# Performance work log

Measured on AMD Instinct MI355X. Metric: run time of the kernel, lower is better.

## Reference

```python
import jax, jax.numpy as jnp
import numpy as np

N_HEADS = 16


def setup_inputs() -> dict:
    key = jax.random.key(0)
    ks = jax.random.split(key, 5)
    B, T, C = 4, 2048, 1024
    return {
        "x": jax.random.normal(ks[0], (B, T, C), dtype=jnp.float32),
        "W_qkv": jax.random.normal(ks[1], (C, 3 * C), dtype=jnp.float32) * 0.02,
        "b_qkv": jax.random.normal(ks[2], (3 * C,), dtype=jnp.float32) * 0.02,
        "W_proj": jax.random.normal(ks[3], (C, C), dtype=jnp.float32) * 0.02,
        "b_proj": jax.random.normal(ks[4], (C,), dtype=jnp.float32) * 0.02,
    }


def reference(x, W_qkv, b_qkv, W_proj, b_proj):
    B, T, C = x.shape
    H = N_HEADS
    hs = C // H
    # QKV projection. NOTE: original reshapes (B,T,3C) -> (B,T,H,3*hs) then
    # chunks last dim, so q/k/v are interleaved per-head slices of the output.
    qkv = x @ W_qkv + b_qkv                       # [B, T, 3C]
    qkv = qkv.reshape(B, T, H, 3 * hs).transpose(0, 2, 1, 3)  # [B, H, T, 3*hs]
    q, k, v = jnp.split(qkv, 3, axis=-1)          # each [B, H, T, hs]
    scale = 1.0 / (hs ** 0.5)
    scores = jnp.einsum("bhqd,bhkd->bhqk", q, k) * scale  # [B, H, T, T]
    causal = jnp.tril(jnp.ones((T, T), dtype=bool))
    scores = jnp.where(causal, scores, jnp.float32(-1e9))
    attn = jax.nn.softmax(scores, axis=-1)
    out = jnp.einsum("bhqk,bhkd->bhqd", attn, v)  # [B, H, T, hs]
    out = out.transpose(0, 2, 1, 3).reshape(B, T, C)
    return out @ W_proj + b_proj
```

## Files before the change

### kernel.cpp

```cpp
#include <hip/hip_runtime.h>

typedef unsigned short u16;
typedef unsigned int u32;
typedef __attribute__((ext_vector_type(8))) short short8;
typedef __attribute__((ext_vector_type(8))) unsigned short u16x8;
typedef __attribute__((ext_vector_type(4))) unsigned short u16x4;
typedef __attribute__((ext_vector_type(2))) unsigned int u32x2;
typedef __attribute__((ext_vector_type(4))) float f32x4;

__device__ __forceinline__ u16 f2bf(float f){
  u32 u = __builtin_bit_cast(u32, f);
  u32 r = u + 0x7FFFu + ((u >> 16) & 1u);
  return (u16)(r >> 16);
}
__device__ __forceinline__ float bf2f(u16 h){
  u32 u = ((u32)h) << 16;
  return __builtin_bit_cast(float, u);
}
__device__ __forceinline__ float f3max(float a, float b, float c){
  return fmaxf(a, fmaxf(b, c));
}
__device__ __forceinline__ u32 cvtpk(float lo, float hi){
  u32 r;
  asm("v_cvt_pk_bf16_f32 %0, %1, %2" : "=v"(r) : "v"(lo), "v"(hi));
  return r;
}

__device__ __forceinline__ void gld_lds16(const u16* g, u16* l){
  __builtin_amdgcn_global_load_lds(
      (const __attribute__((address_space(1))) u32*)g,
      (__attribute__((address_space(3))) u32*)l, 16, 0, 0);
}

#define MFMA(a,b,c) __builtin_amdgcn_mfma_f32_16x16x32_bf16((a),(b),(c),0,0,0)

__global__ void k_cast_x(const float* __restrict__ in, u16* __restrict__ out, int n8){
  int i = blockIdx.x*256 + threadIdx.x;
  if (i >= n8) return;
  const float4 a = ((const float4*)in)[2*i];
  const float4 b = ((const float4*)in)[2*i+1];
  u16x8 o;
  o[0]=f2bf(a.x); o[1]=f2bf(a.y); o[2]=f2bf(a.z); o[3]=f2bf(a.w);
  o[4]=f2bf(b.x); o[5]=f2bf(b.y); o[6]=f2bf(b.z); o[7]=f2bf(b.w);
  ((u16x8*)out)[i] = o;
}

__global__ void k_transpose_cast(const float* __restrict__ in, u16* __restrict__ out,
                                 int R, int C){
  __shared__ float tile[32][33];
  int c0 = blockIdx.x*32, r0 = blockIdx.y*32;
  int tx = threadIdx.x, ty = threadIdx.y;
  #pragma unroll
  for (int i=0;i<4;i++) tile[ty+8*i][tx] = in[(size_t)(r0+ty+8*i)*C + c0+tx];
  __syncthreads();
  #pragma unroll
  for (int i=0;i<4;i++) out[(size_t)(c0+ty+8*i)*R + r0+tx] = f2bf(tile[tx][ty+8*i]);
}

template<int OUT_BF16>
__global__ __launch_bounds__(256) void gemm_bt(const u16* __restrict__ A,
                                               const u16* __restrict__ Bt,
                                               const float* __restrict__ bias,
                                               void* __restrict__ Cp,
                                               int M, int N, int K){
  __shared__ __align__(16) u16 As[128*32];
  __shared__ __align__(16) u16 Bs[128*32];
  int tid = threadIdx.x, lane = tid&63, wv = tid>>6;
  int wr = wv>>1, wc = wv&1;
  int lr16 = lane&15, lg = lane>>4;
  int nwg = gridDim.x*gridDim.y;
  int lin = blockIdx.y*gridDim.x + blockIdx.x;
  int cpx = nwg>>3;
  int swz = (lin&7)*cpx + (lin>>3);
  int bx = swz % gridDim.x, by = swz / gridDim.x;
  size_t brow = (size_t)by*128, bcol = (size_t)bx*128;
  f32x4 acc[4][4] = {};
  int nk = K>>5;
  for (int kt=0; kt<nk; ++kt){
    int k0 = kt*32;
    #pragma unroll
    for (int c=0;c<2;c++){
      gld_lds16(A  + (brow + c*64 + (tid>>2))*K + k0 + (tid&3)*8, &As[c*2048 + tid*8]);
      gld_lds16(Bt + (bcol + c*64 + (tid>>2))*K + k0 + (tid&3)*8, &Bs[c*2048 + tid*8]);
    }
    __syncthreads();
    short8 af[4], bfr[4];
    #pragma unroll
    for (int m=0;m<4;m++) af[m]  = *(const short8*)&As[(wr*64 + m*16 + lr16)*32 + lg*8];
    #pragma unroll
    for (int n=0;n<4;n++) bfr[n] = *(const short8*)&Bs[(wc*64 + n*16 + lr16)*32 + lg*8];
    #pragma unroll
    for (int m=0;m<4;m++)
      #pragma unroll
      for (int n=0;n<4;n++) acc[m][n] = MFMA(af[m], bfr[n], acc[m][n]);
    __syncthreads();
  }
  #pragma unroll
  for (int n=0;n<4;n++){
    size_t col = bcol + wc*64 + n*16 + lr16;
    float bs = bias[col];
    #pragma unroll
    for (int m=0;m<4;m++)
      #pragma unroll
      for (int j=0;j<4;j++){
        size_t row = brow + wr*64 + m*16 + lg*4 + j;
        float v = acc[m][n][j] + bs;
        if (OUT_BF16) ((u16*)Cp)[row*(size_t)N + col] = f2bf(v);
        else          ((float*)Cp)[row*(size_t)N + col] = v;
      }
  }
}

#define G_STAGE(PTR, BROW, LDS, T_, BUF) do{                                   \
  size_t k0_ = (size_t)(T_)*64;                                                \
  _Pragma("unroll")                                                            \
  for (int l=0;l<4;l++){                                                       \
    int r_ = (l&1)*64 + (tid>>3);                                              \
    int h_ = l>>1;                                                             \
    gld_lds16(PTR + (size_t)((BROW) + h_*128 + r_)*1024 + k0_ + (((tid&7)^(r_&7))*8), \
              &LDS[(BUF)*16384 + h_*8192 + (l&1)*4096 + tid*8]);               \
  }                                                                            \
}while(0)

#define RD_A(MQ, CUR) do{                                                      \
  _Pragma("unroll")                                                            \
  for (int m=0;m<4;m++)                                                        \
    _Pragma("unroll")                                                          \
    for (int k=0;k<2;k++){                                                     \
      int hr = (MQ)*64 + m*16 + lr16;                                          \
      af[m][k] = *(const short8*)&Alds[(CUR)*16384 + wr*8192 + hr*64 + (((k*4+lg)^(hr&7))*8)]; \
    }                                                                          \
}while(0)

#define RD_B(NQ, CUR) do{                                                      \
  _Pragma("unroll")                                                            \
  for (int n=0;n<2;n++)                                                        \
    _Pragma("unroll")                                                          \
    for (int k=0;k<2;k++){                                                     \
      int hr = (wc&1)*64 + ((NQ)*2+n)*16 + lr16;                               \
      bfv[(NQ)*2+n][k] = *(const short8*)&Blds[(CUR)*16384 + (wc>>1)*8192 + hr*64 + (((k*4+lg)^(hr&7))*8)]; \
    }                                                                          \
}while(0)

#define MF16(MQ, NQ)                                                           \
  _Pragma("unroll")                                                            \
  for (int k=0;k<2;k++)                                                        \
    _Pragma("unroll")                                                          \
    for (int m=0;m<4;m++)                                                      \
      _Pragma("unroll")                                                        \
      for (int n=0;n<2;n++)                                                    \
        acc[(MQ)*4+m][(NQ)*2+n] = MFMA(af[m][k], bfv[(NQ)*2+n][k], acc[(MQ)*4+m][(NQ)*2+n]);

#define G_TILE(T_, CUR, PF) do{                                                \
  RD_A(0, CUR); RD_B(0, CUR);                                                  \
  if (PF) G_STAGE(Ag, brow, Alds, (T_)+1, (CUR)^1);                            \
  __builtin_amdgcn_s_barrier();                                                \
  __builtin_amdgcn_s_setprio(1); MF16(0,0); __builtin_amdgcn_s_setprio(0);     \
  __builtin_amdgcn_s_barrier();                                                \
  RD_B(1, CUR);                                                                \
  if (PF) G_STAGE(Bg, bcol, Blds, (T_)+1, (CUR)^1);                            \
  __builtin_amdgcn_s_barrier();                                                \
  __builtin_amdgcn_s_setprio(1); MF16(0,1); __builtin_amdgcn_s_setprio(0);     \
  __builtin_amdgcn_s_barrier();                                                \
  RD_A(1, CUR);                                                                \
  __builtin_amdgcn_s_barrier();                                                \
  __builtin_amdgcn_s_setprio(1); MF16(1,1); __builtin_amdgcn_s_setprio(0);     \
  __builtin_amdgcn_s_barrier();                                                \
  __builtin_amdgcn_s_setprio(1); MF16(1,0); __builtin_amdgcn_s_setprio(0);     \
  asm volatile("s_waitcnt vmcnt(0)" ::: "memory");                             \
  __builtin_amdgcn_sched_barrier(0);                                           \
  __builtin_amdgcn_s_barrier();                                                \
}while(0)

__global__ __launch_bounds__(512) void gemm256(const u16* __restrict__ Ag,
                                               const u16* __restrict__ Bg,
                                               const float* __restrict__ bias,
                                               u16* __restrict__ Cp, int N){
  extern __shared__ u16 lds[];
  u16* Alds = lds;
  u16* Blds = lds + 32768;
  int tid = threadIdx.x, lane = tid&63, wid = tid>>6;
  int wr = wid>>2, wc = wid&3;
  int lr16 = lane&15, lg = lane>>4;
  int nbx = gridDim.x;
  int nwg = nbx*gridDim.y;
  int lin = blockIdx.y*nbx + blockIdx.x;
  int cpx = nwg>>3;
  int swz = (lin&7)*cpx + (lin>>3);
  int bx = swz % nbx, by = swz / nbx;
  size_t brow = (size_t)by*256, bcol = (size_t)bx*256;
  f32x4 acc[8][4] = {};
  short8 af[4][2], bfv[4][2];

  G_STAGE(Ag, brow, Alds, 0, 0);
  G_STAGE(Bg, bcol, Blds, 0, 0);
  __syncthreads();

  #pragma unroll 1
  for (int kt=0; kt<16; kt+=2){
    G_TILE(kt,   0, true);
    G_TILE(kt+1, 1, (kt+2<16));
  }

  #pragma unroll
  for (int n=0;n<4;n++){
    size_t col = bcol + wc*64 + n*16 + lr16;
    float bs = bias[col];
    #pragma unroll
    for (int mi=0;mi<8;mi++)
      #pragma unroll
      for (int j=0;j<4;j++){
        size_t row = brow + wr*128 + mi*16 + lg*4 + j;
        Cp[row*(size_t)N + col] = f2bf(acc[mi][n][j] + bs);
      }
  }
}

#define ATTN_ITER(KB, CUR, PF) do{                                             \
  int kv0 = (KB)*64;                                                           \
  if (PF){                                                                     \
    int kv1 = kv0 + 64;                                                        \
    va[0] = *(const u16x4*)(qkv + (bt0 + kv1 + vr0    )*3072 + hq + 128 + vd0);\
    va[1] = *(const u16x4*)(qkv + (bt0 + kv1 + vr0 + 1)*3072 + hq + 128 + vd0);\
    gld_lds16(qkv + (bt0+kv1+kr)*3072 + hq + 64 + kcs, &Ks[(CUR)^1][tid*8]);   \
  }                                                                            \
  f32x4 st[4];                                                                 \
  __builtin_amdgcn_s_setprio(1);                                               \
  _Pragma("unroll")                                                            \
  for (int s=0;s<4;s++){                                                       \
    short8 kf0 = *(const short8*)&Ks[CUR][(s*16+lr16)*64 + ((lg  )^rx)*8];     \
    short8 kf1 = *(const short8*)&Ks[CUR][(s*16+lr16)*64 + ((4+lg)^rx)*8];     \
    f32x4 z = {0,0,0,0};                                                       \
    z = MFMA(kf0, qf[0], z);                                                   \
    z = MFMA(kf1, qf[1], z);                                                   \
    st[s] = z;                                                                 \
  }                                                                            \
  __builtin_amdgcn_s_setprio(0);                                               \
  if (kv0 >= qbase){                                                           \
    _Pragma("unroll")                                                          \
    for (int s=0;s<4;s++)                                                      \
      _Pragma("unroll")                                                        \
      for (int j=0;j<4;j++){                                                   \
        int kvg = kv0 + s*16 + lg*4 + j;                                       \
        if (kvg > qglob) st[s][j] = -1e30f;                                    \
      }                                                                        \
  }                                                                            \
  {                                                                            \
    float mx = f3max(st[0][0], st[0][1], st[0][2]);                            \
    mx = f3max(mx, st[0][3], st[1][0]);                                        \
    mx = f3max(mx, st[1][1], st[1][2]);                                        \
    mx = f3max(mx, st[1][3], st[2][0]);                                        \
    mx = f3max(mx, st[2][1], st[2][2]);                                        \
    mx = f3max(mx, st[2][3], st[3][0]);                                        \
    mx = f3max(mx, st[3][1], st[3][2]);                                        \
    mx = fmaxf(mx, st[3][3]);                                                  \
    mx = fmaxf(mx, __shfl_xor(mx, 16));                                        \
    mx = fmaxf(mx, __shfl_xor(mx, 32));                                        \
    if (__any(mx > m_run + 8.f)){                                              \
      float m_new = fmaxf(m_run, mx);                                          \
      float al = exp2f(m_run - m_new);                                         \
      m_run = m_new;                                                           \
      float arow[4];                                                           \
      _Pragma("unroll")                                                        \
      for (int j=0;j<4;j++) arow[j] = __shfl(al, lg*4 + j);                    \
      _Pragma("unroll")                                                        \
      for (int db=0;db<4;db++)                                                 \
        _Pragma("unroll")                                                      \
        for (int j=0;j<4;j++) O[db][j] *= arow[j];                             \
      _Pragma("unroll")                                                        \
      for (int j=0;j<4;j++) acc_l[j] *= arow[j];                               \
    }                                                                          \
    float mr = m_run;                                                          \
    u32 pw[8];                                                                 \
    _Pragma("unroll")                                                          \
    for (int s=0;s<4;s++){                                                     \
      float p0 = exp2f(st[s][0]-mr), p1 = exp2f(st[s][1]-mr);                  \
      float p2 = exp2f(st[s][2]-mr), p3 = exp2f(st[s][3]-mr);                  \
      pw[s*2+0] = cvtpk(p0,p1);                                                \
      pw[s*2+1] = cvtpk(p2,p3);                                                \
    }                                                                          \
    _Pragma("unroll")                                                          \
    for (int s=0;s<4;s++){                                                     \
      int cp = (s*2 + (lg>>1)) ^ rx;                                           \
      u32x2 w2; w2[0] = pw[s*2]; w2[1] = pw[s*2+1];                            \
      *(u32x2*)&Pl[wv][lr16*64 + cp*8 + (lg&1)*4] = w2;                        \
    }                                                                          \
  }                                                                            \
  if (PF){                                                                     \
    _Pragma("unroll")                                                          \
    for (int k=0;k<4;k++){                                                     \
      int d = vd0+k;                                                           \
      int c = (vr0>>3) ^ (d&7) ^ ((d>>3)&7);                                   \
      u32 w = (u32)va[0][k] | ((u32)va[1][k]<<16);                             \
      *(u32*)&Vt[(CUR)^1][d*64 + c*8 + (vr0&7)] = w;                           \
    }                                                                          \
  }                                                                            \
  __builtin_amdgcn_s_setprio(1);                                               \
  _Pragma("unroll")                                                            \
  for (int B=0;B<2;B++){                                                       \
    short8 pa = *(const short8*)&Pl[wv][lr16*64 + (((B<<2)+lg)^rx)*8];         \
    acc_l = MFMA(pa, onesf, acc_l);                                            \
    _Pragma("unroll")                                                          \
    for (int db=0;db<4;db++){                                                  \
      int d = db*16 + lr16;                                                    \
      short8 vf = *(const short8*)&Vt[CUR][d*64 + ((((B<<2)+lg)^(d&7))^((d>>3)&7))*8]; \
      O[db] = MFMA(pa, vf, O[db]);                                             \
    }                                                                          \
  }                                                                            \
  __builtin_amdgcn_s_setprio(0);                                               \
  __syncthreads();                                                             \
}while(0)

__global__ __launch_bounds__(512, 4) void k_attn(const u16* __restrict__ qkv,
                                                 u16* __restrict__ o, int T){
  __shared__ __align__(16) u16 Ks[2][64*64];
  __shared__ __align__(16) u16 Vt[2][64*64];
  __shared__ __align__(16) u16 Pl[8][16*64];
  int tid = threadIdx.x, lane = tid&63, wv = tid>>6;
  int bh = blockIdx.x;
  int b = bh>>4, h = bh&15;
  int hq = h*192;
  size_t bt0 = (size_t)b*T;
  int lr16 = lane&15, lg = lane>>4;
  int rx = lr16&7;
  int vr0 = (tid>>4)*2, vd0 = (tid&15)*4;
  int kr  = tid>>3;
  int kcs = ((tid&7) ^ (kr&7))*8;
  u16x4 va[2];
  const float QS = 0.18033688f;
  u16x8 ov;
  #pragma unroll
  for (int j=0;j<8;j++) ov[j] = 0x3F80;
  const short8 onesf = __builtin_bit_cast(short8, ov);

  #pragma unroll 1
  for (int half=0; half<2; ++half){
    int qt = half ? (int)blockIdx.y : 15 - (int)blockIdx.y;
    int qbase = qt*128;
    short8 qf[2];
    {
      const u16* qp = qkv + (bt0 + qbase + wv*16 + lr16)*3072 + hq + lg*8;
      #pragma unroll
      for (int t=0;t<2;t++){
        u16x8 v = *(const u16x8*)(qp + t*32);
        #pragma unroll
        for (int j=0;j<8;j++) v[j] = f2bf(bf2f(v[j])*QS);
        qf[t] = __builtin_bit_cast(short8, v);
      }
    }
    f32x4 O[4] = {};
    f32x4 acc_l = {0,0,0,0};
    float m_run = -1e30f;
    int qglob = qbase + wv*16 + lr16;

    {
      va[0] = *(const u16x4*)(qkv + (bt0 + vr0    )*3072 + hq + 128 + vd0);
      va[1] = *(const u16x4*)(qkv + (bt0 + vr0 + 1)*3072 + hq + 128 + vd0);
      gld_lds16(qkv + (bt0+kr)*3072 + hq + 64 + kcs, &Ks[0][tid*8]);
      #pragma unroll
      for (int k=0;k<4;k++){
        int d = vd0+k;
        int c = (vr0>>3) ^ (d&7) ^ ((d>>3)&7);
        u32 w = (u32)va[0][k] | ((u32)va[1][k]<<16);
        *(u32*)&Vt[0][d*64 + c*8 + (vr0&7)] = w;
      }
    }
    __syncthreads();

    int nkv = 2*qt + 2;
    #pragma unroll 1
    for (int kb=0; kb<nkv; kb+=2){
      ATTN_ITER(kb,   0, true);
      ATTN_ITER(kb+1, 1, (kb+2<nkv));
    }
    {
      float lrow[4];
      #pragma unroll
      for (int j=0;j<4;j++) lrow[j] = __builtin_amdgcn_rcpf(acc_l[j]);
      #pragma unroll
      for (int db=0;db<4;db++)
        #pragma unroll
        for (int j=0;j<4;j++){
          size_t row = bt0 + qbase + wv*16 + lg*4 + j;
          o[row*1024 + h*64 + db*16 + lr16] = f2bf(O[db][j] * lrow[j]);
        }
    }
  }
}

extern "C" void kernel_launch(void* const* d_in, const int* in_sizes, int n_in,
                              void* d_out, int out_size, void* d_ws, size_t ws_size,
                              hipStream_t stream){
  (void)in_sizes; (void)n_in; (void)out_size; (void)ws_size;
  const float* x     = (const float*)d_in[0];
  const float* Wqkv  = (const float*)d_in[1];
  const float* bqkv  = (const float*)d_in[2];
  const float* Wproj = (const float*)d_in[3];
  const float* bproj = (const float*)d_in[4];
  float* out = (float*)d_out;
  const int B=4, T=2048, C=1024;
  const int M = B*T;
  char* ws = (char*)d_ws;
  u16* qkvb   = (u16*)(ws);
  u16* attnb  = (u16*)(ws + 50331648);
  u16* xb     = (u16*)(ws + 67108864);
  u16* wqkvT  = (u16*)(ws + 83886080);
  u16* wprojT = (u16*)(ws + 90177536);

  k_cast_x<<<4096, 256, 0, stream>>>(x, xb, M*C/8);
  dim3 tb(32,8);
  k_transpose_cast<<<dim3(96,32), tb, 0, stream>>>(Wqkv, wqkvT, C, 3*C);
  k_transpose_cast<<<dim3(32,32), tb, 0, stream>>>(Wproj, wprojT, C, C);
  gemm256<<<dim3(12,32), 512, 131072, stream>>>(xb, wqkvT, bqkv, qkvb, 3*C);
  k_attn<<<dim3(64,8), 512, 0, stream>>>(qkvb, attnb, T);
  gemm_bt<0><<<dim3(8,64), 256, 0, stream>>>(attnb, wprojT, bproj, out, M, C, C);
}
```

Baseline: 188.3 us.

## Use shared 128x256 pipelined GEMM for QKV and output projections

Replaces the 256x256 QKV GEMM and the simple 128x128 single-buffered projection GEMM with one templated 128x256-tile kernel. It keeps the double-buffered, swizzled LDS pipeline and splits B-tile prefetch into two halves. The kernel requests two blocks per CU via launch bounds and uses less LDS per block, which should improve occupancy and give the projection GEMM the pipelined path. The trade-off is a smaller M tile, which means less reuse per block on the QKV GEMM and more blocks in the grid.

Result: faster. 183.1 us (-2.8%).

```diff
diff --git a/kernel.cpp b/kernel.cpp
--- a/kernel.cpp
+++ b/kernel.cpp
@@ -57,78 +57,33 @@
   for (int i=0;i<4;i++) out[(size_t)(c0+ty+8*i)*R + r0+tx] = f2bf(tile[tx][ty+8*i]);
 }
 
-template<int OUT_BF16>
-__global__ __launch_bounds__(256) void gemm_bt(const u16* __restrict__ A,
-                                               const u16* __restrict__ Bt,
-                                               const float* __restrict__ bias,
-                                               void* __restrict__ Cp,
-                                               int M, int N, int K){
-  __shared__ __align__(16) u16 As[128*32];
-  __shared__ __align__(16) u16 Bs[128*32];
-  int tid = threadIdx.x, lane = tid&63, wv = tid>>6;
-  int wr = wv>>1, wc = wv&1;
-  int lr16 = lane&15, lg = lane>>4;
-  int nwg = gridDim.x*gridDim.y;
-  int lin = blockIdx.y*gridDim.x + blockIdx.x;
-  int cpx = nwg>>3;
-  int swz = (lin&7)*cpx + (lin>>3);
-  int bx = swz % gridDim.x, by = swz / gridDim.x;
-  size_t brow = (size_t)by*128, bcol = (size_t)bx*128;
-  f32x4 acc[4][4] = {};
-  int nk = K>>5;
-  for (int kt=0; kt<nk; ++kt){
-    int k0 = kt*32;
-    #pragma unroll
-    for (int c=0;c<2;c++){
-      gld_lds16(A  + (brow + c*64 + (tid>>2))*K + k0 + (tid&3)*8, &As[c*2048 + tid*8]);
-      gld_lds16(Bt + (bcol + c*64 + (tid>>2))*K + k0 + (tid&3)*8, &Bs[c*2048 + tid*8]);
-    }
-    __syncthreads();
-    short8 af[4], bfr[4];
-    #pragma unroll
-    for (int m=0;m<4;m++) af[m]  = *(const short8*)&As[(wr*64 + m*16 + lr16)*32 + lg*8];
-    #pragma unroll
-    for (int n=0;n<4;n++) bfr[n] = *(const short8*)&Bs[(wc*64 + n*16 + lr16)*32 + lg*8];
-    #pragma unroll
-    for (int m=0;m<4;m++)
-      #pragma unroll
-      for (int n=0;n<4;n++) acc[m][n] = MFMA(af[m], bfr[n], acc[m][n]);
-    __syncthreads();
-  }
-  #pragma unroll
-  for (int n=0;n<4;n++){
-    size_t col = bcol + wc*64 + n*16 + lr16;
-    float bs = bias[col];
-    #pragma unroll
-    for (int m=0;m<4;m++)
-      #pragma unroll
-      for (int j=0;j<4;j++){
-        size_t row = brow + wr*64 + m*16 + lg*4 + j;
-        float v = acc[m][n][j] + bs;
-        if (OUT_BF16) ((u16*)Cp)[row*(size_t)N + col] = f2bf(v);
-        else          ((float*)Cp)[row*(size_t)N + col] = v;
-      }
-  }
-}
-
-#define G_STAGE(PTR, BROW, LDS, T_, BUF) do{                                   \
+#define GS_A(T_, BUF) do{                                                      \
   size_t k0_ = (size_t)(T_)*64;                                                \
   _Pragma("unroll")                                                            \
-  for (int l=0;l<4;l++){                                                       \
-    int r_ = (l&1)*64 + (tid>>3);                                              \
-    int h_ = l>>1;                                                             \
-    gld_lds16(PTR + (size_t)((BROW) + h_*128 + r_)*1024 + k0_ + (((tid&7)^(r_&7))*8), \
-              &LDS[(BUF)*16384 + h_*8192 + (l&1)*4096 + tid*8]);               \
+  for (int l=0;l<2;l++){                                                       \
+    int r_ = l*64 + (tid>>3);                                                  \
+    gld_lds16(Ag + (size_t)(brow + r_)*1024 + k0_ + (((tid&7)^(r_&7))*8),      \
+              &Alds[(BUF)*8192 + l*4096 + tid*8]);                             \
+  }                                                                            \
+}while(0)
+
+#define GS_B(T_, BUF, H_) do{                                                  \
+  size_t k0_ = (size_t)(T_)*64;                                                \
+  _Pragma("unroll")                                                            \
+  for (int l=0;l<2;l++){                                                       \
+    int r_ = (H_)*128 + l*64 + (tid>>3);                                       \
+    gld_lds16(Bg + (size_t)(bcol + r_)*1024 + k0_ + (((tid&7)^(r_&7))*8),      \
+              &Blds[(BUF)*16384 + (H_)*8192 + l*4096 + tid*8]);                \
   }                                                                            \
 }while(0)
 
 #define RD_A(MQ, CUR) do{                                                      \
   _Pragma("unroll")                                                            \
-  for (int m=0;m<4;m++)                                                        \
+  for (int m=0;m<2;m++)                                                        \
     _Pragma("unroll")                                                          \
     for (int k=0;k<2;k++){                                                     \
-      int hr = (MQ)*64 + m*16 + lr16;                                          \
-      af[m][k] = *(const short8*)&Alds[(CUR)*16384 + wr*8192 + hr*64 + (((k*4+lg)^(hr&7))*8)]; \
+      int hr = wr*64 + (MQ)*32 + m*16 + lr16;                                  \
+      af[(MQ)*2+m][k] = *(const short8*)&Alds[(CUR)*8192 + hr*64 + (((k*4+lg)^(hr&7))*8)]; \
     }                                                                          \
 }while(0)
 
@@ -137,48 +92,50 @@
   for (int n=0;n<2;n++)                                                        \
     _Pragma("unroll")                                                          \
     for (int k=0;k<2;k++){                                                     \
-      int hr = (wc&1)*64 + ((NQ)*2+n)*16 + lr16;                               \
-      bfv[(NQ)*2+n][k] = *(const short8*)&Blds[(CUR)*16384 + (wc>>1)*8192 + hr*64 + (((k*4+lg)^(hr&7))*8)]; \
-    }                                                                          \
-}while(0)
-
-#define MF16(MQ, NQ)                                                           \
+      int hr = wc*64 + (NQ)*32 + n*16 + lr16;                                  \
+      bfv[(NQ)*2+n][k] = *(const short8*)&Blds[(CUR)*16384 + hr*64 + (((k*4+lg)^(hr&7))*8)]; \
+    }                                                                          \
+}while(0)
+
+#define MF8(MQ, NQ)                                                            \
   _Pragma("unroll")                                                            \
   for (int k=0;k<2;k++)                                                        \
     _Pragma("unroll")                                                          \
-    for (int m=0;m<4;m++)                                                      \
+    for (int m=0;m<2;m++)                                                      \
       _Pragma("unroll")                                                        \
       for (int n=0;n<2;n++)                                                    \
-        acc[(MQ)*4+m][(NQ)*2+n] = MFMA(af[m][k], bfv[(NQ)*2+n][k], acc[(MQ)*4+m][(NQ)*2+n]);
+        acc[(MQ)*2+m][(NQ)*2+n] = MFMA(af[(MQ)*2+m][k], bfv[(NQ)*2+n][k], acc[(MQ)*2+m][(NQ)*2+n]);
 
 #define G_TILE(T_, CUR, PF) do{                                                \
   RD_A(0, CUR); RD_B(0, CUR);                                                  \
-  if (PF) G_STAGE(Ag, brow, Alds, (T_)+1, (CUR)^1);                            \
-  __builtin_amdgcn_s_barrier();                                                \
-  __builtin_amdgcn_s_setprio(1); MF16(0,0); __builtin_amdgcn_s_setprio(0);     \
+  if (PF) GS_A((T_)+1, (CUR)^1);                                               \
+  __builtin_amdgcn_s_barrier();                                                \
+  __builtin_amdgcn_s_setprio(1); MF8(0,0); __builtin_amdgcn_s_setprio(0);      \
   __builtin_amdgcn_s_barrier();                                                \
   RD_B(1, CUR);                                                                \
-  if (PF) G_STAGE(Bg, bcol, Blds, (T_)+1, (CUR)^1);                            \
-  __builtin_amdgcn_s_barrier();                                                \
-  __builtin_amdgcn_s_setprio(1); MF16(0,1); __builtin_amdgcn_s_setprio(0);     \
+  if (PF) GS_B((T_)+1, (CUR)^1, 0);                                            \
+  __builtin_amdgcn_s_barrier();                                                \
+  __builtin_amdgcn_s_setprio(1); MF8(0,1); __builtin_amdgcn_s_setprio(0);      \
   __builtin_amdgcn_s_barrier();                                                \
   RD_A(1, CUR);                                                                \
-  __builtin_amdgcn_s_barrier();                                                \
-  __builtin_amdgcn_s_setprio(1); MF16(1,1); __builtin_amdgcn_s_setprio(0);     \
-  __builtin_amdgcn_s_barrier();                                                \
-  __builtin_amdgcn_s_setprio(1); MF16(1,0); __builtin_amdgcn_s_setprio(0);     \
+  if (PF) GS_B((T_)+1, (CUR)^1, 1);                                            \
+  __builtin_amdgcn_s_barrier();                                                \
+  __builtin_amdgcn_s_setprio(1); MF8(1,1); __builtin_amdgcn_s_setprio(0);      \
+  __builtin_amdgcn_s_barrier();                                                \
+  __builtin_amdgcn_s_setprio(1); MF8(1,0); __builtin_amdgcn_s_setprio(0);      \
   asm volatile("s_waitcnt vmcnt(0)" ::: "memory");                             \
   __builtin_amdgcn_sched_barrier(0);                                           \
   __builtin_amdgcn_s_barrier();                                                \
 }while(0)
 
-__global__ __launch_bounds__(512) void gemm256(const u16* __restrict__ Ag,
-                                               const u16* __restrict__ Bg,
-                                               const float* __restrict__ bias,
-                                               u16* __restrict__ Cp, int N){
+template<int OUT_BF16>
+__global__ __launch_bounds__(512, 2) void gemm_ph(const u16* __restrict__ Ag,
+                                                  const u16* __restrict__ Bg,
+                                                  const float* __restrict__ bias,
+                                                  void* __restrict__ Cp, int N){
   extern __shared__ u16 lds[];
   u16* Alds = lds;
-  u16* Blds = lds + 32768;
+  u16* Blds = lds + 16384;
   int tid = threadIdx.x, lane = tid&63, wid = tid>>6;
   int wr = wid>>2, wc = wid&3;
   int lr16 = lane&15, lg = lane>>4;
@@ -188,12 +145,13 @@
   int cpx = nwg>>3;
   int swz = (lin&7)*cpx + (lin>>3);
   int bx = swz % nbx, by = swz / nbx;
-  size_t brow = (size_t)by*256, bcol = (size_t)bx*256;
-  f32x4 acc[8][4] = {};
+  size_t brow = (size_t)by*128, bcol = (size_t)bx*256;
+  f32x4 acc[4][4] = {};
   short8 af[4][2], bfv[4][2];
 
-  G_STAGE(Ag, brow, Alds, 0, 0);
-  G_STAGE(Bg, bcol, Blds, 0, 0);
+  GS_A(0, 0);
+  GS_B(0, 0, 0);
+  GS_B(0, 0, 1);
   __syncthreads();
 
   #pragma unroll 1
@@ -203,15 +161,17 @@
   }
 
   #pragma unroll
-  for (int n=0;n<4;n++){
-    size_t col = bcol + wc*64 + n*16 + lr16;
+  for (int ni=0;ni<4;ni++){
+    size_t col = bcol + wc*64 + ni*16 + lr16;
     float bs = bias[col];
     #pragma unroll
-    for (int mi=0;mi<8;mi++)
+    for (int mi=0;mi<4;mi++)
       #pragma unroll
       for (int j=0;j<4;j++){
-        size_t row = brow + wr*128 + mi*16 + lg*4 + j;
-        Cp[row*(size_t)N + col] = f2bf(acc[mi][n][j] + bs);
+        size_t row = brow + wr*64 + mi*16 + lg*4 + j;
+        float v = acc[mi][ni][j] + bs;
+        if (OUT_BF16) ((u16*)Cp)[row*(size_t)N + col] = f2bf(v);
+        else          ((float*)Cp)[row*(size_t)N + col] = v;
       }
   }
 }
@@ -411,7 +371,7 @@
   dim3 tb(32,8);
   k_transpose_cast<<<dim3(96,32), tb, 0, stream>>>(Wqkv, wqkvT, C, 3*C);
   k_transpose_cast<<<dim3(32,32), tb, 0, stream>>>(Wproj, wprojT, C, C);
-  gemm256<<<dim3(12,32), 512, 131072, stream>>>(xb, wqkvT, bqkv, qkvb, 3*C);
+  gemm_ph<1><<<dim3(12,64), 512, 98304, stream>>>(xb, wqkvT, bqkv, qkvb, 3*C);
   k_attn<<<dim3(64,8), 512, 0, stream>>>(qkvb, attnb, T);
-  gemm_bt<0><<<dim3(8,64), 256, 0, stream>>>(attnb, wprojT, bproj, out, M, C, C);
-}
+  gemm_ph<0><<<dim3(4,64), 512, 98304, stream>>>(attnb, wprojT, bproj, out, C);
+}
```
